# Optimization experiments

Hardware: AMD Instinct MI355X
Metric: run time of the kernel (lower is better)

Reference implementation:

```python
import jax, jax.numpy as jnp
import numpy as np

B, N, E = 16, 4096, 65536
CIN, COUT, MAX_DEGREE = 128, 128, 3


def _spmm(rows, cols, vals, x):
    # one sample: y[r] = sum_e vals[e] * x[cols[e]] scattered to rows[e]
    return jax.ops.segment_sum(vals[:, None] * x[cols], rows, num_segments=N)

_spmm_b = jax.vmap(_spmm)  # over batch


def setup_inputs() -> dict:
    key = jax.random.key(0)
    ks = jax.random.split(key, 6)
    x = jax.random.normal(ks[0], (B, N, CIN), dtype=jnp.float32)
    vals = jax.random.normal(ks[1], (B, E), dtype=jnp.float32) * 0.1  # rescaled-Laplacian-like values
    weights = jax.random.normal(ks[2], (MAX_DEGREE + 1, CIN, COUT), dtype=jnp.float32) * 0.1
    bias = jnp.full((COUT,), 0.1, dtype=jnp.float32)
    rows = jax.random.randint(ks[3], (B, E), 0, N, dtype=jnp.int32)
    cols = jax.random.randint(ks[4], (B, E), 0, N, dtype=jnp.int32)
    return {"x": x, "vals": vals, "weights": weights, "bias": bias,
            "rows": rows, "cols": cols}


def reference(x, vals, weights, bias, rows, cols):
    # Chebyshev recursion: T0 = x, T1 = L x, Tk = 2 L T_{k-1} - T_{k-2}
    cheb0 = x
    out = jnp.einsum('bni,io->bno', cheb0, weights[0])
    cheb1 = _spmm_b(rows, cols, vals, x)
    out = out + jnp.einsum('bni,io->bno', cheb1, weights[1])
    for k in range(2, MAX_DEGREE + 1):
        cheb2 = 2.0 * _spmm_b(rows, cols, vals, cheb1) - cheb0
        out = out + jnp.einsum('bni,io->bno', cheb2, weights[k])
        cheb0, cheb1 = cheb1, cheb2
    return jax.nn.relu(out + bias)
```

## Files before the change

### kernel.cpp

```cpp
#include <hip/hip_runtime.h>
#include <hip/hip_bf16.h>
#include <stdint.h>

#define B_ 16
#define N_ 4096
#define E_ 65536
#define C_ 128
#define ECAP 81920

typedef unsigned short u16;
typedef unsigned int u32;
using f32x4 = __attribute__((ext_vector_type(4))) float;
using s16x8 = __attribute__((ext_vector_type(8))) short;

__device__ __forceinline__ u16 f2bf(float f) {
  u32 u = __builtin_bit_cast(u32, f);
  u = (u + 0x7FFFu + ((u >> 16) & 1u)) >> 16;
  return (u16)u;
}
__device__ __forceinline__ float bflo(u32 u) {
  return __builtin_bit_cast(float, u << 16);
}
__device__ __forceinline__ float bfhi(u32 u) {
  return __builtin_bit_cast(float, u & 0xFFFF0000u);
}


__global__ __launch_bounds__(256) void prep_kernel(const float* __restrict__ x,
                                                   u16* __restrict__ xb,
                                                   const float* __restrict__ w,
                                                   u16* __restrict__ wf,
                                                   const int* __restrict__ rows,
                                                   int* __restrict__ hist) {
  int blk = blockIdx.x;
  int t = threadIdx.x;
  if (blk < 4096) {
    int xcd = blk & 7;
    int j   = blk >> 3;
    int b   = xcd * 2 + (j >> 8);
    size_t base = (size_t)b * N_ * C_ + ((j & 255) * 256 + t) * 8;
    const float4* xp = reinterpret_cast<const float4*>(x + base);
    float4 a0 = xp[0];
    float4 a1 = xp[1];
    uint4 p;
    p.x = (u32)f2bf(a0.x) | ((u32)f2bf(a0.y) << 16);
    p.y = (u32)f2bf(a0.z) | ((u32)f2bf(a0.w) << 16);
    p.z = (u32)f2bf(a1.x) | ((u32)f2bf(a1.y) << 16);
    p.w = (u32)f2bf(a1.z) | ((u32)f2bf(a1.w) << 16);
    *reinterpret_cast<uint4*>(xb + base) = p;
  } else if (blk < 4352) {
    int tid = (blk - 4096) * 256 + t;
    int j  = tid & 7;
    int l  = (tid >> 3) & 63;
    int ct = (tid >> 9) & 7;
    int ks = tid >> 12;
    int g  = l >> 4;
    int k  = ks * 32 + g * 8 + j;
    int kk = k >> 7;
    int i  = k & 127;
    int o  = ct * 16 + (l & 15);
    float a = w[(kk * C_ + i) * C_ + o];
    float r;
    if (kk == 0)      r = a - w[(2 * C_ + i) * C_ + o];
    else if (kk == 1) r = a - 3.f * w[(3 * C_ + i) * C_ + o];
    else if (kk == 2) r = 2.f * a;
    else              r = 4.f * a;
    wf[tid] = f2bf(r);
  } else {
    __shared__ int h[N_];
    int hblk = blk - 4352;
    int b = hblk >> 4;
    int c = hblk & 15;
    #pragma unroll
    for (int i = 0; i < 16; ++i) h[t + 256 * i] = 0;
    __syncthreads();
    int ebase = b * E_ + c * 4096;
    #pragma unroll
    for (int i = 0; i < 16; ++i) {
      int r = rows[ebase + t + 256 * i];
      atomicAdd(&h[r], 1);
    }
    __syncthreads();
    int4* hg = reinterpret_cast<int4*>(hist + (size_t)hblk * 4096);
    const int4* hl = reinterpret_cast<const int4*>(h);
    #pragma unroll
    for (int i = 0; i < 4; ++i) hg[t + 256 * i] = hl[t + 256 * i];
  }
}

__global__ __launch_bounds__(256) void rowscan_kernel(int* __restrict__ hist,
                                                      int* __restrict__ cnt) {
  int rg = blockIdx.x * 256 + threadIdx.x;
  int b = rg >> 12;
  int r = rg & 4095;
  int base = (b * 16) * 4096 + r;
  int h[16];
  #pragma unroll
  for (int c = 0; c < 16; ++c) h[c] = hist[base + c * 4096];
  int run = 0;
  #pragma unroll
  for (int c = 0; c < 16; ++c) {
    int v = h[c];
    hist[base + c * 4096] = run;
    run += v;
  }
  cnt[rg] = run;
}

__global__ __launch_bounds__(256) void scan_kernel(const int* __restrict__ cnt,
                                                   int* __restrict__ off) {
  __shared__ int psum[256];
  int b = (blockIdx.x & 7) * 2 + (blockIdx.x >> 3);
  int t = threadIdx.x;
  int local[16];
  int s = 0;
  int base = b * N_ + t * 16;
  #pragma unroll
  for (int i = 0; i < 16; ++i) {
    local[i] = (cnt[base + i] + 3) & ~3;
    s += local[i];
  }
  psum[t] = s;
  __syncthreads();
  if (t == 0) {
    int run = 0;
    for (int i = 0; i < 256; ++i) { int v = psum[i]; psum[i] = run; run += v; }
  }
  __syncthreads();
  int run = psum[t];
  int ob = b * (N_ + 1) + t * 16;
  #pragma unroll
  for (int i = 0; i < 16; ++i) { off[ob + i] = run; run += local[i]; }
  if (t == 255) off[b * (N_ + 1) + N_] = run;
}

__global__ __launch_bounds__(256) void scatter2_kernel(const int* __restrict__ rows,
                                                       const int* __restrict__ cols,
                                                       const float* __restrict__ vals,
                                                       const int* __restrict__ off,
                                                       const int* __restrict__ hist,
                                                       const int* __restrict__ cnt,
                                                       u32* __restrict__ ecv) {
  __shared__ int base[N_];
  __shared__ int cur[N_];
  int xcd = blockIdx.x & 7;
  int j   = blockIdx.x >> 3;
  int b   = xcd * 2 + (j >> 4);
  int c   = j & 15;
  int t   = threadIdx.x;
  const int* hb = hist + (b * 16 + c) * 4096;
  const int* ob = off + b * (N_ + 1);
  #pragma unroll
  for (int i = 0; i < 16; ++i) {
    int idx = t + 256 * i;
    base[idx] = ob[idx] + hb[idx];
    cur[idx] = 0;
  }
  __syncthreads();
  int ebase = b * E_ + c * 4096;
  u32* ecvb = ecv + (size_t)b * ECAP;
  #pragma unroll
  for (int i = 0; i < 16; ++i) {
    int e = ebase + t + 256 * i;
    int r = rows[e];
    int rank = atomicAdd(&cur[r], 1);
    u32 pv = (u32)cols[e] | ((u32)f2bf(vals[e]) << 16);
    ecvb[base[r] + rank] = pv;
  }
  if (c == 0) {
    #pragma unroll
    for (int i = 0; i < 16; ++i) {
      int r = t + 256 * i;
      int real = cnt[b * N_ + r];
      int pbase = ob[r] + real;
      int pad = (-real) & 3;
      for (int k = 0; k < pad; ++k) ecvb[pbase + k] = 0;
    }
  }
}


__global__ __launch_bounds__(256) void spmm_kernel(const u16* __restrict__ src,
                                                   u16* __restrict__ dst,
                                                   const u32* __restrict__ ecv,
                                                   const int* __restrict__ off) {
  int lane = threadIdx.x & 63;
  int wv   = threadIdx.x >> 6;
  int xcd  = blockIdx.x & 7;
  int j    = blockIdx.x >> 3;
  int b    = xcd * 2 + (j >> 9);
  int rp   = ((j & 511) << 2) | wv;
  int eg   = lane >> 4;
  int cl   = lane & 15;
  int n    = rp * 2 + (eg >> 1);
  int sub  = eg & 1;
  int s4 = off[b * (N_ + 1) + n] >> 2;
  int e4 = off[b * (N_ + 1) + n + 1] >> 2;
  const uint4* ecv4 = reinterpret_cast<const uint4*>(ecv + (size_t)b * ECAP);
  const u16* srcb = src + (size_t)b * N_ * C_;
  float acc[8];
  #pragma unroll
  for (int t = 0; t < 8; ++t) acc[t] = 0.f;
  for (int gp = s4 + sub; gp < e4; gp += 2) {
    uint4 cv = ecv4[gp];
    u32 e0 = cv.x, e1 = cv.y, e2 = cv.z, e3 = cv.w;
    uint4 u0 = *reinterpret_cast<const uint4*>(srcb + (size_t)(e0 & 0xFFFFu) * C_ + cl * 8);
    uint4 u1 = *reinterpret_cast<const uint4*>(srcb + (size_t)(e1 & 0xFFFFu) * C_ + cl * 8);
    uint4 u2 = *reinterpret_cast<const uint4*>(srcb + (size_t)(e2 & 0xFFFFu) * C_ + cl * 8);
    uint4 u3 = *reinterpret_cast<const uint4*>(srcb + (size_t)(e3 & 0xFFFFu) * C_ + cl * 8);
    float v0 = bfhi(e0), v1 = bfhi(e1), v2 = bfhi(e2), v3 = bfhi(e3);
    acc[0] = fmaf(v0, bflo(u0.x), acc[0]);
    acc[1] = fmaf(v0, bfhi(u0.x), acc[1]);
    acc[2] = fmaf(v0, bflo(u0.y), acc[2]);
    acc[3] = fmaf(v0, bfhi(u0.y), acc[3]);
    acc[4] = fmaf(v0, bflo(u0.z), acc[4]);
    acc[5] = fmaf(v0, bfhi(u0.z), acc[5]);
    acc[6] = fmaf(v0, bflo(u0.w), acc[6]);
    acc[7] = fmaf(v0, bfhi(u0.w), acc[7]);
    acc[0] = fmaf(v1, bflo(u1.x), acc[0]);
    acc[1] = fmaf(v1, bfhi(u1.x), acc[1]);
    acc[2] = fmaf(v1, bflo(u1.y), acc[2]);
    acc[3] = fmaf(v1, bfhi(u1.y), acc[3]);
    acc[4] = fmaf(v1, bflo(u1.z), acc[4]);
    acc[5] = fmaf(v1, bfhi(u1.z), acc[5]);
    acc[6] = fmaf(v1, bflo(u1.w), acc[6]);
    acc[7] = fmaf(v1, bfhi(u1.w), acc[7]);
    acc[0] = fmaf(v2, bflo(u2.x), acc[0]);
    acc[1] = fmaf(v2, bfhi(u2.x), acc[1]);
    acc[2] = fmaf(v2, bflo(u2.y), acc[2]);
    acc[3] = fmaf(v2, bfhi(u2.y), acc[3]);
    acc[4] = fmaf(v2, bflo(u2.z), acc[4]);
    acc[5] = fmaf(v2, bfhi(u2.z), acc[5]);
    acc[6] = fmaf(v2, bflo(u2.w), acc[6]);
    acc[7] = fmaf(v2, bfhi(u2.w), acc[7]);
    acc[0] = fmaf(v3, bflo(u3.x), acc[0]);
    acc[1] = fmaf(v3, bfhi(u3.x), acc[1]);
    acc[2] = fmaf(v3, bflo(u3.y), acc[2]);
    acc[3] = fmaf(v3, bfhi(u3.y), acc[3]);
    acc[4] = fmaf(v3, bflo(u3.z), acc[4]);
    acc[5] = fmaf(v3, bfhi(u3.z), acc[5]);
    acc[6] = fmaf(v3, bflo(u3.w), acc[6]);
    acc[7] = fmaf(v3, bfhi(u3.w), acc[7]);
  }
  #pragma unroll
  for (int t = 0; t < 8; ++t) acc[t] += __shfl_xor(acc[t], 16);
  if (sub == 0) {
    size_t ro = ((size_t)(b * N_ + n)) * C_ + cl * 8;
    uint4 p;
    p.x = (u32)f2bf(acc[0]) | ((u32)f2bf(acc[1]) << 16);
    p.y = (u32)f2bf(acc[2]) | ((u32)f2bf(acc[3]) << 16);
    p.z = (u32)f2bf(acc[4]) | ((u32)f2bf(acc[5]) << 16);
    p.w = (u32)f2bf(acc[6]) | ((u32)f2bf(acc[7]) << 16);
    *reinterpret_cast<uint4*>(dst + ro) = p;
  }
}


__global__ __launch_bounds__(512) void gemm_kernel(const u16* __restrict__ xb,
                                                   const u16* __restrict__ g1,
                                                   const u16* __restrict__ g2,
                                                   const u16* __restrict__ g3,
                                                   const u16* __restrict__ wf,
                                                   const float* __restrict__ bias,
                                                   float* __restrict__ out) {
  __shared__ u16 wls[65536];
  int tid = threadIdx.x;
  #pragma unroll
  for (int i = 0; i < 16; ++i) {
    int chunk = i * 512 + tid;
    reinterpret_cast<uint4*>(wls)[chunk] = reinterpret_cast<const uint4*>(wf)[chunk];
  }
  __syncthreads();
  int lane = tid & 63;
  int w = tid >> 6;
  int xcd = blockIdx.x & 7;
  int j = blockIdx.x >> 3;
  int b = xcd * 2 + (j >> 4);
  int mb = b * N_ + (j & 15) * 256 + w * 32;
  int g  = lane >> 4;
  int rl = lane & 15;
  const u16* srcs[4] = {xb, g1, g2, g3};
  f32x4 acc0[8], acc1[8];
  #pragma unroll
  for (int t = 0; t < 8; ++t) {
    acc0[t] = (f32x4){0.f, 0.f, 0.f, 0.f};
    acc1[t] = (f32x4){0.f, 0.f, 0.f, 0.f};
  }
  size_t mrow = (size_t)(mb + rl) * C_;
  for (int ks = 0; ks < 16; ++ks) {
    const u16* ap = srcs[ks >> 2] + mrow + (ks & 3) * 32 + g * 8;
    s16x8 a0 = *reinterpret_cast<const s16x8*>(ap);
    s16x8 a1 = *reinterpret_cast<const s16x8*>(ap + 16 * C_);
    const u16* wp = wls + (ks * 8) * 512 + lane * 8;
    #pragma unroll
    for (int ct = 0; ct < 8; ++ct) {
      s16x8 bfv = *reinterpret_cast<const s16x8*>(wp + ct * 512);
      acc0[ct] = __builtin_amdgcn_mfma_f32_16x16x32_bf16(a0, bfv, acc0[ct], 0, 0, 0);
      acc1[ct] = __builtin_amdgcn_mfma_f32_16x16x32_bf16(a1, bfv, acc1[ct], 0, 0, 0);
    }
  }
  #pragma unroll
  for (int ct = 0; ct < 8; ++ct) {
    int o = ct * 16 + rl;
    float bo = bias[o];
    #pragma unroll
    for (int r = 0; r < 4; ++r) {
      int m0 = mb + g * 4 + r;
      int m1 = mb + 16 + g * 4 + r;
      float v0 = acc0[ct][r] + bo;
      float v1 = acc1[ct][r] + bo;
      out[(size_t)m0 * C_ + o] = v0 > 0.f ? v0 : 0.f;
      out[(size_t)m1 * C_ + o] = v1 > 0.f ? v1 : 0.f;
    }
  }
}


extern "C" void kernel_launch(void* const* d_in, const int* in_sizes, int n_in,
                              void* d_out, int out_size, void* d_ws, size_t ws_size,
                              hipStream_t stream) {
  (void)in_sizes; (void)n_in; (void)out_size; (void)ws_size;
  const float* x    = (const float*)d_in[0];
  const float* vals = (const float*)d_in[1];
  const float* wts  = (const float*)d_in[2];
  const float* bias = (const float*)d_in[3];
  const int*   rows = (const int*)d_in[4];
  const int*   cols = (const int*)d_in[5];
  float* out = (float*)d_out;

  const size_t SB = (size_t)B_ * N_ * C_ * sizeof(u16);
  char* ws = (char*)d_ws;
  u16* xb = (u16*)ws;
  u16* g1 = (u16*)(ws + SB);
  u16* g2 = (u16*)(ws + 2 * SB);
  u16* g3 = (u16*)(ws + 3 * SB);
  char* meta = ws + 4 * SB;
  int* hist = (int*)meta;
  u32* ecv  = (u32*)(meta + 4194304);
  int* cnt  = (int*)(meta + 9437184);
  int* off  = (int*)(meta + 9699328);
  u16* wf   = (u16*)(meta + 9961536);

  prep_kernel<<<4608, 256, 0, stream>>>(x, xb, wts, wf, rows, hist);
  rowscan_kernel<<<256, 256, 0, stream>>>(hist, cnt);
  scan_kernel<<<16, 256, 0, stream>>>(cnt, off);
  scatter2_kernel<<<256, 256, 0, stream>>>(rows, cols, vals, off, hist, cnt, ecv);
  spmm_kernel<<<8192, 256, 0, stream>>>(xb, g1, ecv, off);
  spmm_kernel<<<8192, 256, 0, stream>>>(g1, g2, ecv, off);
  spmm_kernel<<<8192, 256, 0, stream>>>(g2, g3, ecv, off);
  gemm_kernel<<<256, 512, 0, stream>>>(xb, g1, g2, g3, wf, bias, out);
}
```

Before: 119.2 us.

## Sub-bucket CSR edges by column range to improve gather locality

The histogram moves out of prep into its own kernel and now bins edges by (row, column>>10), so each row's edges are grouped by which quarter of the source matrix they read. The scatter uses atomic slot counters per bin instead of a separate rank array. The aim is better cache locality for the column gathers in the three SpMM passes. The cost is a histogram four times larger (64 KB of LDS per block), a heavier row scan, and workspace aliasing where hist and cnt reuse the g2/g3 buffers.

```diff
diff --git a/kernel.cpp b/kernel.cpp
--- a/kernel.cpp
+++ b/kernel.cpp
@@ -29,9 +29,7 @@
 __global__ __launch_bounds__(256) void prep_kernel(const float* __restrict__ x,
                                                    u16* __restrict__ xb,
                                                    const float* __restrict__ w,
-                                                   u16* __restrict__ wf,
-                                                   const int* __restrict__ rows,
-                                                   int* __restrict__ hist) {
+                                                   u16* __restrict__ wf) {
   int blk = blockIdx.x;
   int t = threadIdx.x;
   if (blk < 4096) {
@@ -48,7 +46,7 @@
     p.z = (u32)f2bf(a1.x) | ((u32)f2bf(a1.y) << 16);
     p.w = (u32)f2bf(a1.z) | ((u32)f2bf(a1.w) << 16);
     *reinterpret_cast<uint4*>(xb + base) = p;
-  } else if (blk < 4352) {
+  } else {
     int tid = (blk - 4096) * 256 + t;
     int j  = tid & 7;
     int l  = (tid >> 3) & 63;
@@ -66,45 +64,57 @@
     else if (kk == 2) r = 2.f * a;
     else              r = 4.f * a;
     wf[tid] = f2bf(r);
-  } else {
-    __shared__ int h[N_];
-    int hblk = blk - 4352;
-    int b = hblk >> 4;
-    int c = hblk & 15;
-    #pragma unroll
-    for (int i = 0; i < 16; ++i) h[t + 256 * i] = 0;
-    __syncthreads();
-    int ebase = b * E_ + c * 4096;
-    #pragma unroll
-    for (int i = 0; i < 16; ++i) {
-      int r = rows[ebase + t + 256 * i];
-      atomicAdd(&h[r], 1);
-    }
-    __syncthreads();
-    int4* hg = reinterpret_cast<int4*>(hist + (size_t)hblk * 4096);
-    const int4* hl = reinterpret_cast<const int4*>(h);
-    #pragma unroll
-    for (int i = 0; i < 4; ++i) hg[t + 256 * i] = hl[t + 256 * i];
-  }
+  }
+}
+
+
+__global__ __launch_bounds__(256) void hist_kernel(const int* __restrict__ rows,
+                                                   const int* __restrict__ cols,
+                                                   int* __restrict__ hist) {
+  __shared__ int h[16384];
+  int xcd = blockIdx.x & 7;
+  int j   = blockIdx.x >> 3;
+  int b   = xcd * 2 + (j >> 4);
+  int c   = j & 15;
+  int t   = threadIdx.x;
+  int4* hv = reinterpret_cast<int4*>(h);
+  #pragma unroll
+  for (int i = 0; i < 16; ++i) hv[t + 256 * i] = make_int4(0, 0, 0, 0);
+  __syncthreads();
+  int ebase = b * E_ + c * 4096;
+  #pragma unroll
+  for (int i = 0; i < 16; ++i) {
+    int e = ebase + t + 256 * i;
+    int bin = rows[e] * 4 + (cols[e] >> 10);
+    atomicAdd(&h[bin], 1);
+  }
+  __syncthreads();
+  int4* hg = reinterpret_cast<int4*>(hist + ((size_t)(b * 16 + c) << 14));
+  #pragma unroll
+  for (int i = 0; i < 16; ++i) hg[t + 256 * i] = hv[t + 256 * i];
 }
 
 __global__ __launch_bounds__(256) void rowscan_kernel(int* __restrict__ hist,
                                                       int* __restrict__ cnt) {
-  int rg = blockIdx.x * 256 + threadIdx.x;
-  int b = rg >> 12;
-  int r = rg & 4095;
-  int base = (b * 16) * 4096 + r;
-  int h[16];
-  #pragma unroll
-  for (int c = 0; c < 16; ++c) h[c] = hist[base + c * 4096];
+  int xcd = blockIdx.x & 7;
+  int j   = blockIdx.x >> 3;
+  int b   = xcd * 2 + (j >> 4);
+  int rc  = j & 15;
+  int r   = rc * 256 + threadIdx.x;
+  size_t base = (size_t)(b * 16) << 14;
   int run = 0;
   #pragma unroll
-  for (int c = 0; c < 16; ++c) {
-    int v = h[c];
-    hist[base + c * 4096] = run;
-    run += v;
-  }
-  cnt[rg] = run;
+  for (int g = 0; g < 4; ++g) {
+    int bi = r * 4 + g;
+    #pragma unroll
+    for (int c = 0; c < 16; ++c) {
+      size_t idx = base + ((size_t)c << 14) + bi;
+      int v = hist[idx];
+      hist[idx] = run;
+      run += v;
+    }
+  }
+  cnt[b * N_ + r] = run;
 }
 
 __global__ __launch_bounds__(256) void scan_kernel(const int* __restrict__ cnt,
@@ -141,20 +151,18 @@
                                                        const int* __restrict__ hist,
                                                        const int* __restrict__ cnt,
                                                        u32* __restrict__ ecv) {
-  __shared__ int base[N_];
-  __shared__ int cur[N_];
+  __shared__ int base[16384];
   int xcd = blockIdx.x & 7;
   int j   = blockIdx.x >> 3;
   int b   = xcd * 2 + (j >> 4);
   int c   = j & 15;
   int t   = threadIdx.x;
-  const int* hb = hist + (b * 16 + c) * 4096;
+  const int* hb = hist + ((size_t)(b * 16 + c) << 14);
   const int* ob = off + b * (N_ + 1);
   #pragma unroll
-  for (int i = 0; i < 16; ++i) {
-    int idx = t + 256 * i;
-    base[idx] = ob[idx] + hb[idx];
-    cur[idx] = 0;
+  for (int i = 0; i < 64; ++i) {
+    int bin = t + 256 * i;
+    base[bin] = ob[bin >> 2] + hb[bin];
   }
   __syncthreads();
   int ebase = b * E_ + c * 4096;
@@ -163,9 +171,10 @@
   for (int i = 0; i < 16; ++i) {
     int e = ebase + t + 256 * i;
     int r = rows[e];
-    int rank = atomicAdd(&cur[r], 1);
-    u32 pv = (u32)cols[e] | ((u32)f2bf(vals[e]) << 16);
-    ecvb[base[r] + rank] = pv;
+    int col = cols[e];
+    int bin = r * 4 + (col >> 10);
+    int slot = atomicAdd(&base[bin], 1);
+    ecvb[slot] = (u32)col | ((u32)f2bf(vals[e]) << 16);
   }
   if (c == 0) {
     #pragma unroll
@@ -334,14 +343,15 @@
   u16* g1 = (u16*)(ws + SB);
   u16* g2 = (u16*)(ws + 2 * SB);
   u16* g3 = (u16*)(ws + 3 * SB);
+  int* hist = (int*)(ws + 2 * SB);
+  int* cnt  = (int*)(ws + 3 * SB);
   char* meta = ws + 4 * SB;
-  int* hist = (int*)meta;
-  u32* ecv  = (u32*)(meta + 4194304);
-  int* cnt  = (int*)(meta + 9437184);
-  int* off  = (int*)(meta + 9699328);
-  u16* wf   = (u16*)(meta + 9961536);
-
-  prep_kernel<<<4608, 256, 0, stream>>>(x, xb, wts, wf, rows, hist);
+  u32* ecv  = (u32*)meta;
+  int* off  = (int*)(meta + 5242880);
+  u16* wf   = (u16*)(meta + 5505088);
+
+  prep_kernel<<<4352, 256, 0, stream>>>(x, xb, wts, wf);
+  hist_kernel<<<256, 256, 0, stream>>>(rows, cols, hist);
   rowscan_kernel<<<256, 256, 0, stream>>>(hist, cnt);
   scan_kernel<<<16, 256, 0, stream>>>(cnt, off);
   scatter2_kernel<<<256, 256, 0, stream>>>(rows, cols, vals, off, hist, cnt, ecv);
```

After: 129.6 us. 1.09x slower.
